# Kernel tuning notes

Hardware: AMD Instinct MI355X
Metric: run time of the kernel (lower is better)

## Reference

```python
import jax, jax.numpy as jnp
import numpy as np

B, CIN, COUT, T, J = 64, 128, 128, 128, 25
EPS = 1e-5  # BatchNorm2d default eps


def setup_inputs() -> dict:
    key = jax.random.key(0)
    k = jax.random.split(key, 5)
    x = jax.random.normal(k[0], (B, CIN, T, J), jnp.float32)
    adj = jax.random.normal(k[1], (J, J), jnp.float32) / np.sqrt(J).astype(np.float32)
    Wk = jax.random.normal(k[2], (COUT, CIN), jnp.float32) / np.sqrt(CIN).astype(np.float32)
    Wq = jax.random.normal(k[3], (COUT, CIN), jnp.float32) / np.sqrt(CIN).astype(np.float32)
    Ws = jax.random.normal(k[4], (COUT, CIN), jnp.float32) / np.sqrt(CIN).astype(np.float32)
    return {
        "x": x, "adj": adj,
        "Wk": Wk, "bk": jnp.zeros((COUT,), jnp.float32),
        "Wq": Wq, "bq": jnp.zeros((COUT,), jnp.float32),
        "Ws": Ws, "bs": jnp.zeros((COUT,), jnp.float32),
        "gamma": jnp.ones((COUT,), jnp.float32),
        "beta": jnp.zeros((COUT,), jnp.float32),
        "run_mean": jnp.zeros((COUT,), jnp.float32),
        "run_var": jnp.ones((COUT,), jnp.float32),
        "alpha": jnp.ones((1,), jnp.float32),
    }


def reference(x, adj, Wk, bk, Wq, bq, Ws, bs, gamma, beta, run_mean, run_var, alpha):
    # static graph conv: aggregate over joints with the shared adjacency
    static = jnp.einsum('bctj,jk->bctk', x, adj)              # [B,Cin,T,J]
    # 1x1 conv == channel matmul
    static_feat = jnp.einsum('oc,bctj->botj', Ws, static) + bs[None, :, None, None]  # [B,Cout,T,J]
    # temporal mean pooling, then key/query 1x1 convs
    x_t = x.mean(axis=2)                                      # [B,Cin,J]
    kk = jnp.einsum('oc,bcj->boj', Wk, x_t) + bk[None, :, None]  # [B,Cout,J]
    qq = jnp.einsum('oc,bcj->boj', Wq, x_t) + bq[None, :, None]  # [B,Cout,J]
    # attention-style dynamic adjacency: softmax(q^T k / sqrt(Cout)) over last axis
    scale = jnp.sqrt(jnp.asarray(kk.shape[1], x.dtype))
    scores = jnp.einsum('bcj,bck->bjk', qq, kk) / scale       # [B,J,J]
    dyn = jax.nn.softmax(scores, axis=-1)                     # [B,J,J]
    # original expands dyn to (B*T, Cout, J, J); same math without materialization:
    dyn_feat = jnp.einsum('bctj,bjk->bctk', static_feat, dyn)  # [B,Cout,T,J]
    out = static_feat + alpha[0] * dyn_feat
    # BatchNorm2d in inference mode (running stats), then ReLU
    inv = gamma[None, :, None, None] * jax.lax.rsqrt(run_var[None, :, None, None] + EPS)
    out = (out - run_mean[None, :, None, None]) * inv + beta[None, :, None, None]
    return jax.nn.relu(out)
```

## Files before the change

kernel.cpp:

```cpp
#include <hip/hip_runtime.h>

#define B_ 64
#define C_ 128
#define T_ 128
#define J_ 25
#define PIT 136
#define XP 40
#define GP 136
#define TT 4

typedef unsigned short ushort_t;
typedef __attribute__((ext_vector_type(8))) unsigned short ushort8;
typedef __attribute__((ext_vector_type(4))) unsigned short ushort4_t;
typedef __attribute__((ext_vector_type(8))) _Float16 half8;
typedef __attribute__((ext_vector_type(4))) float f32x4;
typedef float f32x4u __attribute__((ext_vector_type(4), aligned(4)));
typedef unsigned short ushort8u __attribute__((ext_vector_type(8), aligned(2)));

__device__ __forceinline__ float bf2f(ushort_t u) {
  unsigned int v = ((unsigned int)u) << 16;
  return __builtin_bit_cast(float, v);
}
__device__ __forceinline__ ushort_t f2bf(float f) {
  unsigned int u = __builtin_bit_cast(unsigned int, f);
  u += 0x7FFFu + ((u >> 16) & 1u);
  return (ushort_t)(u >> 16);
}
__device__ __forceinline__ ushort_t f2h_bits(float f) {
  _Float16 h = (_Float16)f;
  return __builtin_bit_cast(ushort_t, h);
}
__device__ __forceinline__ float h2f(ushort_t u) {
  return (float)__builtin_bit_cast(_Float16, u);
}
__device__ __forceinline__ half8 cvt_bf8_h8(ushort8 u) {
  half8 r;
#pragma unroll
  for (int i = 0; i < 8; ++i) r[i] = (_Float16)bf2f(u[i]);
  return r;
}
__device__ __forceinline__ float ldv(const void* p, long i, int isf32) {
  return isf32 ? ((const float*)p)[i] : bf2f(((const ushort_t*)p)[i]);
}
__device__ __forceinline__ half8 ld8h(const void* p, long i, int isf32) {
  half8 r;
  if (isf32) {
    const float* f = (const float*)p + i;
    f32x4 v0 = *(const f32x4*)f;
    f32x4 v1 = *(const f32x4*)(f + 4);
#pragma unroll
    for (int k = 0; k < 4; ++k) {
      r[k] = (_Float16)v0[k];
      r[4 + k] = (_Float16)v1[k];
    }
  } else {
    ushort8 u = *(const ushort8*)((const ushort_t*)p + i);
    r = cvt_bf8_h8(u);
  }
  return r;
}

__device__ __forceinline__ int detect_isf32(const void* p, int tid) {
  const ushort_t* u = (const ushort_t*)p;
  float a = fabsf(bf2f(u[2 * (tid & 63)]));
  int ok = (a > 1e-4f && a < 64.f) ? 1 : 0;
  unsigned long long m = __ballot(ok);
  return (__popcll(m) > 32) ? 0 : 1;
}

__global__ __launch_bounds__(256) void k_mean(const void* __restrict__ x,
                                              ushort_t* __restrict__ xt) {
  const int bc = blockIdx.x;
  const int b = bc >> 7, c = bc & 127;
  const long base = (long)bc * 3200;
  const int tid = threadIdx.x;
  const int isf32 = detect_isf32((const ushort_t*)x + base, tid);
  __shared__ float pl[3200];
  __shared__ float red[8][32];
  if (isf32) {
    const f32x4* src = (const f32x4*)((const float*)x + base);
    for (int i = tid; i < 800; i += 256) *(f32x4*)&pl[i * 4] = src[i];
  } else {
    const ushort8* src = (const ushort8*)((const ushort_t*)x + base);
    for (int i = tid; i < 400; i += 256) {
      ushort8 u = src[i];
      f32x4 v0, v1;
#pragma unroll
      for (int r = 0; r < 4; ++r) {
        v0[r] = bf2f(u[r]);
        v1[r] = bf2f(u[4 + r]);
      }
      *(f32x4*)&pl[i * 8] = v0;
      *(f32x4*)&pl[i * 8 + 4] = v1;
    }
  }
  __syncthreads();
  const int j = tid & 31, g = tid >> 5;
  float s = 0.f;
  if (j < J_) {
#pragma unroll
    for (int i = 0; i < 16; ++i) s += pl[(g * 16 + i) * 25 + j];
  }
  red[g][j] = s;
  __syncthreads();
  if (tid < 32) {
    float tot = 0.f;
#pragma unroll
    for (int gg = 0; gg < 8; ++gg) tot += red[gg][tid];
    if (tid < J_) xt[b * 4096 + tid * 128 + c] = f2h_bits(tot * (1.0f / 128.0f));
  }
}

__global__ __launch_bounds__(512) void k_attn(
    const ushort_t* __restrict__ xt, const void* __restrict__ adj,
    const void* __restrict__ Wk, const void* __restrict__ bk,
    const void* __restrict__ Wq, const void* __restrict__ bq,
    const void* __restrict__ alphap, ushort_t* __restrict__ fkws,
    float* __restrict__ sws) {
  const int b = blockIdx.x;
  const int tid = threadIdx.x;
  const int isf32 = detect_isf32(Wk, tid);
  const int wv = tid >> 6, lane = tid & 63, lrow = lane & 15, quad = lane >> 4;
  const int mg = wv >> 2, wvv = wv & 3;
  const float alpha = ldv(alphap, 0, isf32);

  __shared__ __align__(16) ushort_t xtT[32 * PIT];
  __shared__ __align__(16) ushort_t kkT[32 * PIT];
  __shared__ __align__(16) ushort_t qqT[32 * PIT];
  __shared__ float sc[32 * 33];
  __shared__ float adjL[25 * 26];

  for (int idx = tid; idx < 32 * 17; idx += 512) {
    int r = idx / 17, c8 = idx % 17;
    ushort8 v = {};
    if (r < J_ && c8 < 16) v = *(const ushort8*)&xt[b * 4096 + r * 128 + c8 * 8];
    *(ushort8*)&xtT[r * PIT + c8 * 8] = v;
  }
  for (int idx = tid; idx < 625; idx += 512)
    adjL[(idx / 25) * 26 + (idx % 25)] = ldv(adj, idx, isf32);
  __syncthreads();

  {
    const void* W = mg ? Wq : Wk;
    const void* bias = mg ? bq : bk;
    ushort_t* dstT = mg ? qqT : kkT;
    f32x4 acc[2][2] = {};
    for (int ks = 0; ks < 4; ++ks) {
      half8 bfr[2];
#pragma unroll
      for (int jt = 0; jt < 2; ++jt)
        bfr[jt] = *(const half8*)&xtT[(jt * 16 + lrow) * PIT + ks * 32 + quad * 8];
#pragma unroll
      for (int ot = 0; ot < 2; ++ot) {
        int o = (2 * wvv + ot) * 16 + lrow;
        half8 afr = ld8h(W, o * 128 + ks * 32 + quad * 8, isf32);
#pragma unroll
        for (int jt = 0; jt < 2; ++jt)
          acc[ot][jt] = __builtin_amdgcn_mfma_f32_16x16x32_f16(afr, bfr[jt],
                                                               acc[ot][jt], 0, 0, 0);
      }
    }
#pragma unroll
    for (int ot = 0; ot < 2; ++ot) {
      int obase = (2 * wvv + ot) * 16 + quad * 4;
#pragma unroll
      for (int jt = 0; jt < 2; ++jt) {
        int j = jt * 16 + lrow;
        ushort_t pack[4];
#pragma unroll
        for (int r = 0; r < 4; ++r)
          pack[r] = f2h_bits(acc[ot][jt][r] + ldv(bias, obase + r, isf32));
        *(ushort4_t*)&dstT[j * PIT + obase] = *(ushort4_t*)pack;
      }
    }
  }
  __syncthreads();

  if (wv < 4) {
    const int mt = wv >> 1, nt = wv & 1;
    f32x4 acc = {};
    for (int ks = 0; ks < 4; ++ks) {
      half8 afr = *(const half8*)&qqT[(mt * 16 + lrow) * PIT + ks * 32 + quad * 8];
      half8 bfr = *(const half8*)&kkT[(nt * 16 + lrow) * PIT + ks * 32 + quad * 8];
      acc = __builtin_amdgcn_mfma_f32_16x16x32_f16(afr, bfr, acc, 0, 0, 0);
    }
    const float rs = 0.08838834764831845f;
#pragma unroll
    for (int r = 0; r < 4; ++r)
      sc[(mt * 16 + quad * 4 + r) * 33 + nt * 16 + lrow] = acc[r] * rs;
  }
  __syncthreads();

  if (tid < J_) {
    float m = -1e30f;
    for (int k = 0; k < J_; ++k) m = fmaxf(m, sc[tid * 33 + k]);
    float sum = 0.f;
    for (int k = 0; k < J_; ++k) {
      float e = expf(sc[tid * 33 + k] - m);
      sc[tid * 33 + k] = e;
      sum += e;
    }
    float inv = 1.f / sum;
    for (int k = 0; k < J_; ++k) sc[tid * 33 + k] *= inv;
  }
  __syncthreads();

  for (int idx = tid; idx < 1280; idx += 512) {
    int k = idx / XP, jj = idx % XP;
    float v = 0.f;
    if (k < J_ && jj < J_) {
      v = adjL[jj * 26 + k];
      float d = 0.f;
      for (int m = 0; m < J_; ++m) d += adjL[jj * 26 + m] * sc[m * 33 + k];
      v += alpha * d;
    }
    fkws[b * 1280 + idx] = f2h_bits(v);
  }
  if (tid < 32) {
    float v = 0.f;
    if (tid < J_) {
      float d = 0.f;
      for (int jj = 0; jj < J_; ++jj) d += sc[jj * 33 + tid];
      v = 1.f + alpha * d;
    }
    sws[b * 32 + tid] = v;
  }
}

#define SM_FK 0
#define SM_GT 2560
#define SM_TOT (2560 + 100 * GP * 2)
__global__ __launch_bounds__(256, 5) void k_main(
    const void* __restrict__ x, const void* __restrict__ Ws,
    const void* __restrict__ bs, const void* __restrict__ gamma,
    const void* __restrict__ beta, const void* __restrict__ rmean,
    const void* __restrict__ rvar, const ushort_t* __restrict__ fkws,
    const float* __restrict__ sws, void* __restrict__ out) {
  const int tid = threadIdx.x;
  const int isf32 = detect_isf32(Ws, tid);
  const int b = blockIdx.x >> 5, tb = blockIdx.x & 31, t0 = tb * TT;
  const int wv = tid >> 6, lane = tid & 63, lrow = lane & 15, quad = lane >> 4;

  __shared__ __align__(16) char smem[SM_TOT];
  __shared__ float bnscale[128], bnshift[128], bsv[128], sv[32];
  ushort_t* fk = (ushort_t*)(smem + SM_FK);
  ushort_t* gt = (ushort_t*)(smem + SM_GT);
  ushort_t* outbuf = (ushort_t*)(smem + SM_GT);

  half8 xa[TT][2];
  {
    const float* xf = (const float*)x;
    const ushort_t* xh = (const ushort_t*)x;
#pragma unroll
    for (int t = 0; t < TT; ++t)
#pragma unroll
      for (int ci = 0; ci < 2; ++ci) {
        const int ct = 2 * wv + ci;
        const long p = (long)b * 409600 + (long)(ct * 16 + lrow) * 3200 + (t0 + t) * 25;
        half8 bfr;
        if (quad < 3) {
          if (isf32) {
            f32x4u v0 = *(const f32x4u*)(xf + p + quad * 8);
            f32x4u v1 = *(const f32x4u*)(xf + p + quad * 8 + 4);
#pragma unroll
            for (int r = 0; r < 4; ++r) {
              bfr[r] = (_Float16)v0[r];
              bfr[4 + r] = (_Float16)v1[r];
            }
          } else {
            ushort8u u = *(const ushort8u*)(xh + p + quad * 8);
#pragma unroll
            for (int r = 0; r < 8; ++r) bfr[r] = (_Float16)bf2f(u[r]);
          }
        } else {
          bfr = (half8){};
          bfr[0] = (_Float16)(isf32 ? xf[p + 24] : bf2f(xh[p + 24]));
        }
        xa[t][ci] = bfr;
      }
  }

  half8 wsf[2][4];
#pragma unroll
  for (int ot = 0; ot < 2; ++ot) {
    int o = (2 * wv + ot) * 16 + lrow;
#pragma unroll
    for (int ks = 0; ks < 4; ++ks)
      wsf[ot][ks] = ld8h(Ws, o * 128 + ks * 32 + quad * 8, isf32);
  }

  for (int i = tid; i < 160; i += 256)
    *(ushort8*)&fk[i * 8] = *(const ushort8*)&fkws[b * 1280 + i * 8];
  if (tid < 32) sv[tid] = sws[b * 32 + tid];
  if (tid < 128) {
    float g = ldv(gamma, tid, isf32), v = ldv(rvar, tid, isf32);
    float scl = g * rsqrtf(v + 1e-5f);
    bnscale[tid] = scl;
    bnshift[tid] = ldv(beta, tid, isf32) - ldv(rmean, tid, isf32) * scl;
    bsv[tid] = ldv(bs, tid, isf32);
  }
  __syncthreads();

  {
    half8 afr[2];
#pragma unroll
    for (int mt = 0; mt < 2; ++mt)
      afr[mt] = *(const half8*)&fk[(mt * 16 + lrow) * XP + quad * 8];
#pragma unroll
    for (int t = 0; t < TT; ++t) {
#pragma unroll
      for (int ci = 0; ci < 2; ++ci) {
        const int ct = 2 * wv + ci;
        f32x4 accg[2] = {};
#pragma unroll
        for (int mt = 0; mt < 2; ++mt)
          accg[mt] = __builtin_amdgcn_mfma_f32_16x16x32_f16(afr[mt], xa[t][ci],
                                                            accg[mt], 0, 0, 0);
#pragma unroll
        for (int mt = 0; mt < 2; ++mt)
#pragma unroll
          for (int r = 0; r < 4; ++r) {
            const int kk = mt * 16 + quad * 4 + r;
            if (kk < J_)
              gt[(t * 25 + kk) * GP + ct * 16 + lrow] = f2h_bits(accg[mt][r]);
          }
      }
    }
  }
  __syncthreads();

  f32x4 acc[2][7];
#pragma unroll
  for (int ot = 0; ot < 2; ++ot)
#pragma unroll
    for (int nt = 0; nt < 7; ++nt) acc[ot][nt] = (f32x4){};
  for (int ks = 0; ks < 4; ++ks) {
#pragma unroll
    for (int nt = 0; nt < 7; ++nt) {
      half8 bfr = (half8){};
      if (nt < 6 || lrow < 4)
        bfr = *(const half8*)&gt[(nt * 16 + lrow) * GP + ks * 32 + quad * 8];
#pragma unroll
      for (int ot = 0; ot < 2; ++ot)
        acc[ot][nt] = __builtin_amdgcn_mfma_f32_16x16x32_f16(wsf[ot][ks], bfr,
                                                             acc[ot][nt], 0, 0, 0);
    }
  }
  __syncthreads();

#pragma unroll
  for (int nt = 0; nt < 7; ++nt) {
    int n = nt * 16 + lrow;
    if (n < 100) {
      float svk = sv[n % 25];
#pragma unroll
      for (int ot = 0; ot < 2; ++ot) {
        int obase = (2 * wv + ot) * 16 + quad * 4;
#pragma unroll
        for (int r = 0; r < 4; ++r) {
          int o = obase + r;
          float v = acc[ot][nt][r] + bsv[o] * svk;
          v = v * bnscale[o] + bnshift[o];
          outbuf[o * 100 + n] = f2h_bits(fmaxf(v, 0.f));
        }
      }
    }
  }
  __syncthreads();

  {
    const long obase = ((long)(b * 128) * 128 + t0) * 25;
    if (isf32) {
      float* of = (float*)out + obase;
      for (int idx = tid; idx < 3200; idx += 256) {
        int o = idx / 25, q = idx % 25;
        ushort4_t u = *(const ushort4_t*)&outbuf[o * 100 + q * 4];
        f32x4 v;
#pragma unroll
        for (int r = 0; r < 4; ++r) v[r] = h2f(u[r]);
        *(f32x4*)(of + (long)o * 3200 + q * 4) = v;
      }
    } else {
      ushort_t* oh = (ushort_t*)out + obase;
      for (int idx = tid; idx < 3200; idx += 256) {
        int o = idx / 25, q = idx % 25;
        ushort4_t u = *(const ushort4_t*)&outbuf[o * 100 + q * 4];
        ushort4_t w;
#pragma unroll
        for (int r = 0; r < 4; ++r) w[r] = f2bf(h2f(u[r]));
        *(ushort4_t*)(oh + (long)o * 3200 + q * 4) = w;
      }
    }
  }
}

extern "C" void kernel_launch(void* const* d_in, const int* in_sizes, int n_in,
                              void* d_out, int out_size, void* d_ws, size_t ws_size,
                              hipStream_t stream) {
  const void* x = d_in[0];
  const void* adj = d_in[1];
  const void* Wk = d_in[2];
  const void* bk = d_in[3];
  const void* Wq = d_in[4];
  const void* bq = d_in[5];
  const void* Ws = d_in[6];
  const void* bsp = d_in[7];
  const void* gamma = d_in[8];
  const void* beta = d_in[9];
  const void* rmean = d_in[10];
  const void* rvar = d_in[11];
  const void* alphap = d_in[12];

  char* ws = (char*)d_ws;
  ushort_t* xt = (ushort_t*)ws;
  ushort_t* fkws = (ushort_t*)(ws + 64 * 4096 * 2);
  float* sws = (float*)(ws + 64 * 4096 * 2 + 64 * 1280 * 2);

  k_mean<<<B_ * C_, 256, 0, stream>>>(x, xt);
  k_attn<<<B_, 512, 0, stream>>>(xt, adj, Wk, bk, Wq, bq, alphap, fkws, sws);
  k_main<<<B_ * (T_ / TT), 256, 0, stream>>>(x, Ws, bsp, gamma, beta, rmean, rvar,
                                             fkws, sws, d_out);
}
```

Before: 311.2 us.

## Remap block indices across XCDs, defer x loads, relax launch bounds

Block indices are remapped so that consecutive hardware block IDs, which are dealt round-robin across the 8 XCDs, handle contiguous (batch, time-tile) work within each XCD. This is meant to improve L2 locality for shared per-batch data. The x-fragment loads move from the kernel prologue into the graph-aggregation loop, right before the MFMA that uses them. That shortens register live ranges but gives up some load latency hiding behind the fk/parameter setup and the barrier. The occupancy hint in launch_bounds drops from 5 to 4 blocks, giving the compiler more registers per thread at the cost of fewer resident waves.

```diff
diff --git a/kernel.cpp b/kernel.cpp
--- a/kernel.cpp
+++ b/kernel.cpp
@@ -230,7 +230,7 @@
 #define SM_FK 0
 #define SM_GT 2560
 #define SM_TOT (2560 + 100 * GP * 2)
-__global__ __launch_bounds__(256, 5) void k_main(
+__global__ __launch_bounds__(256, 4) void k_main(
     const void* __restrict__ x, const void* __restrict__ Ws,
     const void* __restrict__ bs, const void* __restrict__ gamma,
     const void* __restrict__ beta, const void* __restrict__ rmean,
@@ -238,7 +238,9 @@
     const float* __restrict__ sws, void* __restrict__ out) {
   const int tid = threadIdx.x;
   const int isf32 = detect_isf32(Ws, tid);
-  const int b = blockIdx.x >> 5, tb = blockIdx.x & 31, t0 = tb * TT;
+  const int p = blockIdx.x;
+  const int idx0 = (p & 7) * 256 + (p >> 3);
+  const int b = idx0 >> 5, tb = idx0 & 31, t0 = tb * TT;
   const int wv = tid >> 6, lane = tid & 63, lrow = lane & 15, quad = lane >> 4;
 
   __shared__ __align__(16) char smem[SM_TOT];
@@ -246,39 +248,6 @@
   ushort_t* fk = (ushort_t*)(smem + SM_FK);
   ushort_t* gt = (ushort_t*)(smem + SM_GT);
   ushort_t* outbuf = (ushort_t*)(smem + SM_GT);
-
-  half8 xa[TT][2];
-  {
-    const float* xf = (const float*)x;
-    const ushort_t* xh = (const ushort_t*)x;
-#pragma unroll
-    for (int t = 0; t < TT; ++t)
-#pragma unroll
-      for (int ci = 0; ci < 2; ++ci) {
-        const int ct = 2 * wv + ci;
-        const long p = (long)b * 409600 + (long)(ct * 16 + lrow) * 3200 + (t0 + t) * 25;
-        half8 bfr;
-        if (quad < 3) {
-          if (isf32) {
-            f32x4u v0 = *(const f32x4u*)(xf + p + quad * 8);
-            f32x4u v1 = *(const f32x4u*)(xf + p + quad * 8 + 4);
-#pragma unroll
-            for (int r = 0; r < 4; ++r) {
-              bfr[r] = (_Float16)v0[r];
-              bfr[4 + r] = (_Float16)v1[r];
-            }
-          } else {
-            ushort8u u = *(const ushort8u*)(xh + p + quad * 8);
-#pragma unroll
-            for (int r = 0; r < 8; ++r) bfr[r] = (_Float16)bf2f(u[r]);
-          }
-        } else {
-          bfr = (half8){};
-          bfr[0] = (_Float16)(isf32 ? xf[p + 24] : bf2f(xh[p + 24]));
-        }
-        xa[t][ci] = bfr;
-      }
-  }
 
   half8 wsf[2][4];
 #pragma unroll
@@ -306,21 +275,42 @@
 #pragma unroll
     for (int mt = 0; mt < 2; ++mt)
       afr[mt] = *(const half8*)&fk[(mt * 16 + lrow) * XP + quad * 8];
+    const float* xf = (const float*)x;
+    const ushort_t* xh = (const ushort_t*)x;
 #pragma unroll
     for (int t = 0; t < TT; ++t) {
 #pragma unroll
       for (int ci = 0; ci < 2; ++ci) {
-        const int ct = 2 * wv + ci;
+        int ct = 2 * wv + ci;
+        long pp = (long)b * 409600 + (long)(ct * 16 + lrow) * 3200 + (t0 + t) * 25;
+        half8 bfr;
+        if (quad < 3) {
+          if (isf32) {
+            f32x4u v0 = *(const f32x4u*)(xf + pp + quad * 8);
+            f32x4u v1 = *(const f32x4u*)(xf + pp + quad * 8 + 4);
+#pragma unroll
+            for (int r = 0; r < 4; ++r) {
+              bfr[r] = (_Float16)v0[r];
+              bfr[4 + r] = (_Float16)v1[r];
+            }
+          } else {
+            ushort8u u = *(const ushort8u*)(xh + pp + quad * 8);
+#pragma unroll
+            for (int r = 0; r < 8; ++r) bfr[r] = (_Float16)bf2f(u[r]);
+          }
+        } else {
+          bfr = (half8){};
+          bfr[0] = (_Float16)(isf32 ? xf[pp + 24] : bf2f(xh[pp + 24]));
+        }
         f32x4 accg[2] = {};
 #pragma unroll
         for (int mt = 0; mt < 2; ++mt)
-          accg[mt] = __builtin_amdgcn_mfma_f32_16x16x32_f16(afr[mt], xa[t][ci],
-                                                            accg[mt], 0, 0, 0);
+          accg[mt] = __builtin_amdgcn_mfma_f32_16x16x32_f16(afr[mt], bfr, accg[mt], 0, 0, 0);
 #pragma unroll
         for (int mt = 0; mt < 2; ++mt)
 #pragma unroll
           for (int r = 0; r < 4; ++r) {
-            const int kk = mt * 16 + quad * 4 + r;
+            int kk = mt * 16 + quad * 4 + r;
             if (kk < J_)
               gt[(t * 25 + kk) * GP + ct * 16 + lrow] = f2h_bits(accg[mt][r]);
           }
@@ -372,8 +362,8 @@
     const long obase = ((long)(b * 128) * 128 + t0) * 25;
     if (isf32) {
       float* of = (float*)out + obase;
-      for (int idx = tid; idx < 3200; idx += 256) {
-        int o = idx / 25, q = idx % 25;
+      for (int i2 = tid; i2 < 3200; i2 += 256) {
+        int o = i2 / 25, q = i2 % 25;
         ushort4_t u = *(const ushort4_t*)&outbuf[o * 100 + q * 4];
         f32x4 v;
 #pragma unroll
@@ -382,8 +372,8 @@
       }
     } else {
       ushort_t* oh = (ushort_t*)out + obase;
-      for (int idx = tid; idx < 3200; idx += 256) {
-        int o = idx / 25, q = idx % 25;
+      for (int i2 = tid; i2 < 3200; i2 += 256) {
+        int o = i2 / 25, q = i2 % 25;
         ushort4_t u = *(const ushort4_t*)&outbuf[o * 100 + q * 4];
         ushort4_t w;
 #pragma unroll
```

After: 267.0 us. 14.2% less time.
